# Performance work log

Hardware: AMD Instinct MI355X
Metric: run time of the kernel (lower is better)

## Reference

```python
import jax, jax.numpy as jnp
import numpy as np

N, IN_DIM, OUT_DIM, HEADS, E = 50000, 256, 256, 4, 800000
HEAD_DIM = OUT_DIM // HEADS
NEG_SLOPE = 0.2


def setup_inputs() -> dict:
    key = jax.random.key(0)
    k = jax.random.split(key, 6)
    h = jax.random.normal(k[0], (N, IN_DIM), dtype=jnp.float32)
    edge_index = jax.random.randint(k[1], (2, E), 0, N, dtype=jnp.int32)
    # xavier-uniform-ish scales
    W = jax.random.normal(k[2], (OUT_DIM, IN_DIM), dtype=jnp.float32) * (1.0 / np.sqrt(IN_DIM))
    b = jnp.zeros((OUT_DIM,), dtype=jnp.float32)
    a_src = jax.random.normal(k[3], (HEADS, HEAD_DIM), dtype=jnp.float32) * (1.0 / np.sqrt(HEAD_DIM))
    a_dst = jax.random.normal(k[4], (HEADS, HEAD_DIM), dtype=jnp.float32) * (1.0 / np.sqrt(HEAD_DIM))
    return {"h": h, "edge_index": edge_index, "W": W, "b": b, "a_src": a_src, "a_dst": a_dst}


def reference(h, edge_index, W, b, a_src, a_dst):
    idx_i, idx_j = edge_index[0], edge_index[1]
    Wh = (h @ W.T + b).reshape(N, HEADS, HEAD_DIM)  # [N,H,D]
    # per-node attention logits components (avoids gathering full Wh per edge twice)
    alpha_src = jnp.einsum('nhd,hd->nh', Wh, a_src)  # [N,H]
    alpha_dst = jnp.einsum('nhd,hd->nh', Wh, a_dst)  # [N,H]
    e = jax.nn.leaky_relu(alpha_src[idx_i] + alpha_dst[idx_j], NEG_SLOPE)  # [E,H]
    # segment softmax over neighbors j of each destination row i (sparse.softmax dim=1)
    m = jax.ops.segment_max(e, idx_i, num_segments=N)  # [N,H]
    ex = jnp.exp(e - m[idx_i])
    denom = jax.ops.segment_sum(ex, idx_i, num_segments=N)  # [N,H]
    att = ex / denom[idx_i]  # [E,H]
    # sparse-mm aggregation: out_i = sum_j att_ij * Wh_j, per head
    out = jax.ops.segment_sum(att[:, :, None] * Wh[idx_j], idx_i, num_segments=N)  # [N,H,D]
    return out.reshape(N, OUT_DIM)
```

## Files before the change

kernel.cpp:

```cpp
#include <hip/hip_runtime.h>
#include <hip/hip_bf16.h>
#include <stdint.h>

constexpr int IN_DIM  = 256;
constexpr int OUT_DIM = 256;
constexpr int HEADS   = 4;
constexpr int HEAD_DIM = 64;
constexpr float NEG_SLOPE = 0.2f;

typedef __attribute__((ext_vector_type(8))) short bf16x8;
typedef __attribute__((ext_vector_type(4))) float f32x4;

static __device__ __forceinline__ unsigned short f2bf(float f) {
  union { float f; uint32_t u; } v; v.f = f;
  uint32_t u = v.u;
  return (unsigned short)((u + 0x7fffu + ((u >> 16) & 1u)) >> 16);
}

__global__ __launch_bounds__(256) void k_prep(
    const float* __restrict__ W, const float* __restrict__ b,
    const float* __restrict__ a_src, const float* __restrict__ a_dst,
    float* __restrict__ csrc, unsigned short* __restrict__ Wb,
    int* __restrict__ counts, int* __restrict__ cursor, int N) {
  int bid = blockIdx.x, t = threadIdx.x;
  int i = bid * 256 + t;
  if (i < N) { counts[i] = 0; cursor[i] = 0; }
  if (bid == 0 && t < 8) {
    int hh = t & 3;
    const float* a = (t < 4 ? a_src : a_dst) + hh * HEAD_DIM;
    float cs = 0.f;
    for (int d = 0; d < HEAD_DIM; ++d) cs += b[hh * HEAD_DIM + d] * a[d];
    csrc[t] = cs;
  } else if (bid >= 8 && bid < 40) {
    int base = (bid - 8) * 2048 + t * 8;
    float4 f0 = *(const float4*)(W + base);
    float4 f1 = *(const float4*)(W + base + 4);
    union { unsigned short us[8]; uint4 u4; } pk;
    pk.us[0]=f2bf(f0.x); pk.us[1]=f2bf(f0.y); pk.us[2]=f2bf(f0.z); pk.us[3]=f2bf(f0.w);
    pk.us[4]=f2bf(f1.x); pk.us[5]=f2bf(f1.y); pk.us[6]=f2bf(f1.z); pk.us[7]=f2bf(f1.w);
    *(uint4*)(Wb + base) = pk.u4;
  }
}

__global__ __launch_bounds__(256) void k_gemm_mfma(
    const float* __restrict__ h, const unsigned short* __restrict__ Wb,
    const float* __restrict__ b,
    const float* __restrict__ a_src, const float* __restrict__ a_dst,
    const float* __restrict__ csrc,
    unsigned short* __restrict__ Wh,
    float* __restrict__ asrc, float* __restrict__ adst, int N) {
  __shared__ unsigned short lds[2 * 20480];
  const int t = threadIdx.x;
  const int w = t >> 6, l = t & 63;
  const int lm = l & 15, g = l >> 4;
  const int r0 = blockIdx.x * 64;

  f32x4 acc[4][4];
  const f32x4 fz = {0.f, 0.f, 0.f, 0.f};
#pragma unroll
  for (int fm = 0; fm < 4; ++fm)
#pragma unroll
    for (int fn = 0; fn < 4; ++fn) acc[fm][fn] = fz;

  float breg[4], asg[4], adg[4];
#pragma unroll
  for (int fn = 0; fn < 4; ++fn) {
    breg[fn] = b[w * 64 + fn * 16 + lm];
    asg[fn]  = a_src[w * 64 + fn * 16 + lm];
    adg[fn]  = a_dst[w * 64 + fn * 16 + lm];
  }

  auto stageA = [&](int ch, int s) {
    int k0 = ch * 64;
    int row = t >> 2;
    int grow = r0 + row;
    unsigned short* dstbase = lds + s * 20480 + row * 64;
#pragma unroll
    for (int cc = 0; cc < 2; ++cc) {
      int c = (t & 3) * 2 + cc;
      union { unsigned short us[8]; bf16x8 v; } pk;
      if (grow < N) {
        const float* src = h + (size_t)grow * 256 + k0 + c * 8;
        float4 f0 = *(const float4*)(src);
        float4 f1 = *(const float4*)(src + 4);
        pk.us[0]=f2bf(f0.x); pk.us[1]=f2bf(f0.y); pk.us[2]=f2bf(f0.z); pk.us[3]=f2bf(f0.w);
        pk.us[4]=f2bf(f1.x); pk.us[5]=f2bf(f1.y); pk.us[6]=f2bf(f1.z); pk.us[7]=f2bf(f1.w);
      } else {
#pragma unroll
        for (int e = 0; e < 8; ++e) pk.us[e] = 0;
      }
      *(bf16x8*)(dstbase + ((c ^ (row & 7)) * 8)) = pk.v;
    }
  };

  auto stageB = [&](int ch, int s) {
    int k0 = ch * 64;
    unsigned short* Bbase = lds + s * 20480 + 4096;
    int c  = l & 7;
    int rs = l >> 3;
#pragma unroll
    for (int i = 0; i < 8; ++i) {
      int row = w * 64 + i * 8 + rs;
      bf16x8 v = *(const bf16x8*)(Wb + (size_t)row * 256 + k0 + c * 8);
      *(bf16x8*)(Bbase + row * 64 + ((c ^ rs) * 8)) = v;
    }
  };

  auto compute = [&](int s) {
    const unsigned short* A = lds + s * 20480;
    const unsigned short* B = lds + s * 20480 + 4096;
#pragma unroll
    for (int ks = 0; ks < 2; ++ks) {
      bf16x8 af[4], bfr[4];
#pragma unroll
      for (int fm = 0; fm < 4; ++fm) {
        int row = fm * 16 + lm;
        af[fm] = *(const bf16x8*)(A + row * 64 + (((ks * 4 + g) ^ (row & 7)) * 8));
      }
#pragma unroll
      for (int fn = 0; fn < 4; ++fn) {
        int row = w * 64 + fn * 16 + lm;
        bfr[fn] = *(const bf16x8*)(B + row * 64 + (((ks * 4 + g) ^ (row & 7)) * 8));
      }
#pragma unroll
      for (int fm = 0; fm < 4; ++fm)
#pragma unroll
        for (int fn = 0; fn < 4; ++fn)
          acc[fm][fn] = __builtin_amdgcn_mfma_f32_16x16x32_bf16(
              af[fm], bfr[fn], acc[fm][fn], 0, 0, 0);
    }
  };

  stageA(0, 0); stageB(0, 0);
  __syncthreads();
#pragma unroll
  for (int ch = 0; ch < 4; ++ch) {
    int cur = ch & 1;
    if (ch < 3) { stageA(ch + 1, cur ^ 1); stageB(ch + 1, cur ^ 1); }
    compute(cur);
    __syncthreads();
  }

#pragma unroll
  for (int fm = 0; fm < 4; ++fm) {
#pragma unroll
    for (int r = 0; r < 4; ++r) {
      int grow = r0 + fm * 16 + g * 4 + r;
      if (grow < N) {
        size_t rowoff = (size_t)grow * 256;
#pragma unroll
        for (int fn = 0; fn < 4; ++fn) {
          int col = w * 64 + fn * 16 + lm;
          Wh[rowoff + col] = f2bf(acc[fm][fn][r] + breg[fn]);
        }
      }
    }
  }

  float cs = csrc[w], cd = csrc[4 + w];
#pragma unroll
  for (int fm = 0; fm < 4; ++fm) {
#pragma unroll
    for (int r = 0; r < 4; ++r) {
      float ps = acc[fm][0][r] * asg[0] + acc[fm][1][r] * asg[1]
               + acc[fm][2][r] * asg[2] + acc[fm][3][r] * asg[3];
      float pd = acc[fm][0][r] * adg[0] + acc[fm][1][r] * adg[1]
               + acc[fm][2][r] * adg[2] + acc[fm][3][r] * adg[3];
#pragma unroll
      for (int off = 1; off < 16; off <<= 1) {
        ps += __shfl_xor(ps, off, 64);
        pd += __shfl_xor(pd, off, 64);
      }
      if (lm == 0) {
        int grow = r0 + fm * 16 + g * 4 + r;
        if (grow < N) {
          asrc[grow * 4 + w] = ps + cs;
          adst[grow * 4 + w] = pd + cd;
        }
      }
    }
  }
}

__global__ __launch_bounds__(256) void k_hist(const int* __restrict__ idx_i,
                                              int* __restrict__ counts, int E) {
  int e = blockIdx.x * 256 + threadIdx.x;
  if (e < E) atomicAdd(&counts[idx_i[e]], 1);
}

__global__ __launch_bounds__(256) void k_scanA(const int* __restrict__ counts,
                                               int* __restrict__ offsets,
                                               int* __restrict__ bsum, int N) {
  __shared__ int s[256];
  int t = threadIdx.x;
  int idx = blockIdx.x * 256 + t;
  int v = (idx < N) ? counts[idx] : 0;
  s[t] = v;
  __syncthreads();
  for (int off = 1; off < 256; off <<= 1) {
    int x = (t >= off) ? s[t - off] : 0;
    __syncthreads();
    s[t] += x;
    __syncthreads();
  }
  if (idx < N) offsets[idx] = s[t] - v;
  if (t == 255) bsum[blockIdx.x] = s[255];
}

__global__ __launch_bounds__(256) void k_scanB(int* __restrict__ bsum, int nb) {
  __shared__ int s[256];
  int t = threadIdx.x;
  int v = (t < nb) ? bsum[t] : 0;
  s[t] = v;
  __syncthreads();
  for (int off = 1; off < 256; off <<= 1) {
    int x = (t >= off) ? s[t - off] : 0;
    __syncthreads();
    s[t] += x;
    __syncthreads();
  }
  if (t < nb) bsum[t] = s[t] - v;
}

__global__ __launch_bounds__(256) void k_scanC(int* __restrict__ offsets,
                                               const int* __restrict__ bsum,
                                               int N, int E) {
  int idx = blockIdx.x * 256 + threadIdx.x;
  if (idx < N) offsets[idx] += bsum[blockIdx.x];
  if (idx == 0) offsets[N] = E;
}

__global__ __launch_bounds__(256) void k_scatter(const int* __restrict__ idx_i,
                                                 const int* __restrict__ idx_j,
                                                 const int* __restrict__ offsets,
                                                 int* __restrict__ cursor,
                                                 int* __restrict__ csr_j, int E) {
  int e = blockIdx.x * 256 + threadIdx.x;
  if (e < E) {
    int i = idx_i[e];
    int p = offsets[i] + atomicAdd(&cursor[i], 1);
    csr_j[p] = idx_j[e];
  }
}

__global__ __launch_bounds__(256) void k_aggregate(const int* __restrict__ offsets,
                                                   const int* __restrict__ csr_j,
                                                   const float* __restrict__ asrc,
                                                   const float* __restrict__ adst,
                                                   const unsigned short* __restrict__ Wh,
                                                   float* __restrict__ out, int N) {
  int t = threadIdx.x;
  int wv = t >> 6, l = t & 63;
  int half = l >> 5, ll = l & 31;
  int i = blockIdx.x * 8 + wv * 2 + half;
  bool valid = i < N;
  int beg = valid ? offsets[i] : 0;
  int end = valid ? offsets[i + 1] : 0;
  int deg = end - beg;
  int hh = ll >> 3;
  float aih = valid ? asrc[i * 4 + hh] : 0.f;

  float o[8];
#pragma unroll
  for (int d = 0; d < 8; ++d) o[d] = 0.f;
  float denom = 0.f;

  for (int q = 0; q < deg; q += 8) {
    int jj[8];
    float wgt[8];
    uint4 vv[8];
#pragma unroll
    for (int k = 0; k < 8; ++k) {
      int qk = q + k;
      int qc = qk < deg - 1 ? qk : deg - 1;
      jj[k] = csr_j[beg + qc];
    }
#pragma unroll
    for (int k = 0; k < 8; ++k) {
      float s = aih + adst[(size_t)jj[k] * 4 + hh];
      s = s > 0.f ? s : NEG_SLOPE * s;
      s = (q + k < deg) ? s : -1e38f;
      wgt[k] = __expf(s);
      vv[k] = *(const uint4*)(Wh + (size_t)jj[k] * 256 + ll * 8);
    }
    denom += ((wgt[0] + wgt[1]) + (wgt[2] + wgt[3])) +
             ((wgt[4] + wgt[5]) + (wgt[6] + wgt[7]));
#pragma unroll
    for (int k = 0; k < 8; ++k) {
      union { uint32_t u; float f; } c0, c1, c2, c3, c4, c5, c6, c7;
      c0.u = vv[k].x << 16; c1.u = vv[k].x & 0xffff0000u;
      c2.u = vv[k].y << 16; c3.u = vv[k].y & 0xffff0000u;
      c4.u = vv[k].z << 16; c5.u = vv[k].z & 0xffff0000u;
      c6.u = vv[k].w << 16; c7.u = vv[k].w & 0xffff0000u;
      float wk = wgt[k];
      o[0] += wk * c0.f; o[1] += wk * c1.f;
      o[2] += wk * c2.f; o[3] += wk * c3.f;
      o[4] += wk * c4.f; o[5] += wk * c5.f;
      o[6] += wk * c6.f; o[7] += wk * c7.f;
    }
  }

  if (valid) {
    float inv = (deg > 0) ? 1.f / denom : 0.f;
    float4 o0 = {o[0] * inv, o[1] * inv, o[2] * inv, o[3] * inv};
    float4 o1 = {o[4] * inv, o[5] * inv, o[6] * inv, o[7] * inv};
    float* dst = out + (size_t)i * 256 + ll * 8;
    *(float4*)(dst) = o0;
    *(float4*)(dst + 4) = o1;
  }
}

extern "C" void kernel_launch(void* const* d_in, const int* in_sizes, int n_in,
                              void* d_out, int out_size, void* d_ws, size_t ws_size,
                              hipStream_t stream) {
  const float* h     = (const float*)d_in[0];
  const int*   eidx  = (const int*)  d_in[1];
  const float* W     = (const float*)d_in[2];
  const float* b     = (const float*)d_in[3];
  const float* a_src = (const float*)d_in[4];
  const float* a_dst = (const float*)d_in[5];
  float* out = (float*)d_out;

  const int N = in_sizes[0] / IN_DIM;
  const int E = in_sizes[1] / 2;
  const int* idx_i = eidx;
  const int* idx_j = eidx + E;

  char* p = (char*)d_ws;
  auto alloc = [&](size_t bytes) {
    char* r = p;
    p += (bytes + 255) & ~(size_t)255;
    return r;
  };
  float* csrc = (float*)alloc(8 * sizeof(float));
  unsigned short* Wb = (unsigned short*)alloc((size_t)OUT_DIM * IN_DIM * sizeof(unsigned short));
  unsigned short* Wh = (unsigned short*)alloc((size_t)N * OUT_DIM * sizeof(unsigned short));
  float* asrc = (float*)alloc((size_t)N * HEADS * sizeof(float));
  float* adst = (float*)alloc((size_t)N * HEADS * sizeof(float));
  int* counts  = (int*)alloc((size_t)N * sizeof(int));
  int* offsets = (int*)alloc(((size_t)N + 1) * sizeof(int));
  int* cursor  = (int*)alloc((size_t)N * sizeof(int));
  int* bsum    = (int*)alloc(256 * sizeof(int));
  int* csrj    = (int*)alloc((size_t)E * sizeof(int));

  const int nbN = (N + 255) / 256;
  const int nbE = (E + 255) / 256;

  k_prep<<<nbN, 256, 0, stream>>>(W, b, a_src, a_dst, csrc, Wb, counts, cursor, N);
  k_gemm_mfma<<<(N + 63) / 64, 256, 0, stream>>>(h, Wb, b, a_src, a_dst, csrc,
                                                 Wh, asrc, adst, N);
  k_hist<<<nbE, 256, 0, stream>>>(idx_i, counts, E);
  k_scanA<<<nbN, 256, 0, stream>>>(counts, offsets, bsum, N);
  k_scanB<<<1, 256, 0, stream>>>(bsum, nbN);
  k_scanC<<<nbN, 256, 0, stream>>>(offsets, bsum, N, E);
  k_scatter<<<nbE, 256, 0, stream>>>(idx_i, idx_j, offsets, cursor, csrj, E);
  k_aggregate<<<(N + 7) / 8, 256, 0, stream>>>(offsets, csrj, asrc, adst, Wh, out, N);
}
```

Baseline: 187.2 us.

## Fuse histogram into GEMM, merge scan phases, use offsets as scatter cursor

```diff
diff --git a/kernel.cpp b/kernel.cpp
--- a/kernel.cpp
+++ b/kernel.cpp
@@ -20,25 +20,22 @@
 __global__ __launch_bounds__(256) void k_prep(
     const float* __restrict__ W, const float* __restrict__ b,
     const float* __restrict__ a_src, const float* __restrict__ a_dst,
-    float* __restrict__ csrc, unsigned short* __restrict__ Wb,
-    int* __restrict__ counts, int* __restrict__ cursor, int N) {
+    float* __restrict__ csrc, unsigned short* __restrict__ Wb) {
   int bid = blockIdx.x, t = threadIdx.x;
-  int i = bid * 256 + t;
-  if (i < N) { counts[i] = 0; cursor[i] = 0; }
-  if (bid == 0 && t < 8) {
-    int hh = t & 3;
-    const float* a = (t < 4 ? a_src : a_dst) + hh * HEAD_DIM;
-    float cs = 0.f;
-    for (int d = 0; d < HEAD_DIM; ++d) cs += b[hh * HEAD_DIM + d] * a[d];
-    csrc[t] = cs;
-  } else if (bid >= 8 && bid < 40) {
-    int base = (bid - 8) * 2048 + t * 8;
+  if (bid < 32) {
+    int base = bid * 2048 + t * 8;
     float4 f0 = *(const float4*)(W + base);
     float4 f1 = *(const float4*)(W + base + 4);
     union { unsigned short us[8]; uint4 u4; } pk;
     pk.us[0]=f2bf(f0.x); pk.us[1]=f2bf(f0.y); pk.us[2]=f2bf(f0.z); pk.us[3]=f2bf(f0.w);
     pk.us[4]=f2bf(f1.x); pk.us[5]=f2bf(f1.y); pk.us[6]=f2bf(f1.z); pk.us[7]=f2bf(f1.w);
     *(uint4*)(Wb + base) = pk.u4;
+  } else if (t < 8) {
+    int hh = t & 3;
+    const float* a = (t < 4 ? a_src : a_dst) + hh * HEAD_DIM;
+    float cs = 0.f;
+    for (int d = 0; d < HEAD_DIM; ++d) cs += b[hh * HEAD_DIM + d] * a[d];
+    csrc[t] = cs;
   }
 }
 
@@ -48,7 +45,8 @@
     const float* __restrict__ a_src, const float* __restrict__ a_dst,
     const float* __restrict__ csrc,
     unsigned short* __restrict__ Wh,
-    float* __restrict__ asrc, float* __restrict__ adst, int N) {
+    float* __restrict__ asrc, float* __restrict__ adst,
+    const int* __restrict__ idx_i, int* __restrict__ counts, int N, int E) {
   __shared__ unsigned short lds[2 * 20480];
   const int t = threadIdx.x;
   const int w = t >> 6, l = t & 63;
@@ -80,9 +78,9 @@
       int c = (t & 3) * 2 + cc;
       union { unsigned short us[8]; bf16x8 v; } pk;
       if (grow < N) {
-        const float* src = h + (size_t)grow * 256 + k0 + c * 8;
-        float4 f0 = *(const float4*)(src);
-        float4 f1 = *(const float4*)(src + 4);
+        const f32x4* src = (const f32x4*)(h + (size_t)grow * 256 + k0 + c * 8);
+        f32x4 f0 = __builtin_nontemporal_load(src);
+        f32x4 f1 = __builtin_nontemporal_load(src + 1);
         pk.us[0]=f2bf(f0.x); pk.us[1]=f2bf(f0.y); pk.us[2]=f2bf(f0.z); pk.us[3]=f2bf(f0.w);
         pk.us[4]=f2bf(f1.x); pk.us[5]=f2bf(f1.y); pk.us[6]=f2bf(f1.z); pk.us[7]=f2bf(f1.w);
       } else {
@@ -180,12 +178,14 @@
       }
     }
   }
-}
-
-__global__ __launch_bounds__(256) void k_hist(const int* __restrict__ idx_i,
-                                              int* __restrict__ counts, int E) {
-  int e = blockIdx.x * 256 + threadIdx.x;
-  if (e < E) atomicAdd(&counts[idx_i[e]], 1);
+
+  {
+    long long nb = gridDim.x;
+    long long e0 = (long long)blockIdx.x * E / nb;
+    long long e1 = ((long long)blockIdx.x + 1) * E / nb;
+    for (long long e = e0 + t; e < e1; e += 256)
+      atomicAdd(&counts[idx_i[e]], 1);
+  }
 }
 
 __global__ __launch_bounds__(256) void k_scanA(const int* __restrict__ counts,
@@ -207,7 +207,9 @@
   if (t == 255) bsum[blockIdx.x] = s[255];
 }
 
-__global__ __launch_bounds__(256) void k_scanB(int* __restrict__ bsum, int nb) {
+__global__ __launch_bounds__(256) void k_scanBC(int* __restrict__ offsets,
+                                                const int* __restrict__ bsum,
+                                                int nb, int N) {
   __shared__ int s[256];
   int t = threadIdx.x;
   int v = (t < nb) ? bsum[t] : 0;
@@ -219,26 +221,20 @@
     s[t] += x;
     __syncthreads();
   }
-  if (t < nb) bsum[t] = s[t] - v;
-}
-
-__global__ __launch_bounds__(256) void k_scanC(int* __restrict__ offsets,
-                                               const int* __restrict__ bsum,
-                                               int N, int E) {
-  int idx = blockIdx.x * 256 + threadIdx.x;
-  if (idx < N) offsets[idx] += bsum[blockIdx.x];
-  if (idx == 0) offsets[N] = E;
+  int bid = blockIdx.x;
+  int add = (bid > 0) ? s[bid - 1] : 0;
+  int idx = bid * 256 + t;
+  if (idx < N) offsets[idx] += add;
 }
 
 __global__ __launch_bounds__(256) void k_scatter(const int* __restrict__ idx_i,
                                                  const int* __restrict__ idx_j,
-                                                 const int* __restrict__ offsets,
-                                                 int* __restrict__ cursor,
+                                                 int* __restrict__ offsets,
                                                  int* __restrict__ csr_j, int E) {
   int e = blockIdx.x * 256 + threadIdx.x;
   if (e < E) {
     int i = idx_i[e];
-    int p = offsets[i] + atomicAdd(&cursor[i], 1);
+    int p = atomicAdd(&offsets[i], 1);
     csr_j[p] = idx_j[e];
   }
 }
@@ -254,8 +250,8 @@
   int half = l >> 5, ll = l & 31;
   int i = blockIdx.x * 8 + wv * 2 + half;
   bool valid = i < N;
-  int beg = valid ? offsets[i] : 0;
-  int end = valid ? offsets[i + 1] : 0;
+  int beg = (valid && i > 0) ? offsets[i - 1] : 0;
+  int end = valid ? offsets[i] : 0;
   int deg = end - beg;
   int hh = ll >> 3;
   float aih = valid ? asrc[i * 4 + hh] : 0.f;
@@ -302,11 +298,11 @@
 
   if (valid) {
     float inv = (deg > 0) ? 1.f / denom : 0.f;
-    float4 o0 = {o[0] * inv, o[1] * inv, o[2] * inv, o[3] * inv};
-    float4 o1 = {o[4] * inv, o[5] * inv, o[6] * inv, o[7] * inv};
-    float* dst = out + (size_t)i * 256 + ll * 8;
-    *(float4*)(dst) = o0;
-    *(float4*)(dst + 4) = o1;
+    f32x4 o0 = {o[0] * inv, o[1] * inv, o[2] * inv, o[3] * inv};
+    f32x4 o1 = {o[4] * inv, o[5] * inv, o[6] * inv, o[7] * inv};
+    f32x4* dst = (f32x4*)(out + (size_t)i * 256 + ll * 8);
+    __builtin_nontemporal_store(o0, dst);
+    __builtin_nontemporal_store(o1, dst + 1);
   }
 }
 
@@ -339,20 +335,19 @@
   float* adst = (float*)alloc((size_t)N * HEADS * sizeof(float));
   int* counts  = (int*)alloc((size_t)N * sizeof(int));
   int* offsets = (int*)alloc(((size_t)N + 1) * sizeof(int));
-  int* cursor  = (int*)alloc((size_t)N * sizeof(int));
   int* bsum    = (int*)alloc(256 * sizeof(int));
   int* csrj    = (int*)alloc((size_t)E * sizeof(int));
 
   const int nbN = (N + 255) / 256;
   const int nbE = (E + 255) / 256;
-
-  k_prep<<<nbN, 256, 0, stream>>>(W, b, a_src, a_dst, csrc, Wb, counts, cursor, N);
-  k_gemm_mfma<<<(N + 63) / 64, 256, 0, stream>>>(h, Wb, b, a_src, a_dst, csrc,
-                                                 Wh, asrc, adst, N);
-  k_hist<<<nbE, 256, 0, stream>>>(idx_i, counts, E);
+  const int nbM = (N + 63) / 64;
+
+  (void)hipMemsetAsync(counts, 0, (size_t)N * sizeof(int), stream);
+  k_prep<<<33, 256, 0, stream>>>(W, b, a_src, a_dst, csrc, Wb);
+  k_gemm_mfma<<<nbM, 256, 0, stream>>>(h, Wb, b, a_src, a_dst, csrc,
+                                       Wh, asrc, adst, idx_i, counts, N, E);
   k_scanA<<<nbN, 256, 0, stream>>>(counts, offsets, bsum, N);
-  k_scanB<<<1, 256, 0, stream>>>(bsum, nbN);
-  k_scanC<<<nbN, 256, 0, stream>>>(offsets, bsum, N, E);
-  k_scatter<<<nbE, 256, 0, stream>>>(idx_i, idx_j, offsets, cursor, csrj, E);
+  k_scanBC<<<nbN, 256, 0, stream>>>(offsets, bsum, nbN, N);
+  k_scatter<<<nbE, 256, 0, stream>>>(idx_i, idx_j, offsets, csrj, E);
   k_aggregate<<<(N + 7) / 8, 256, 0, stream>>>(offsets, csrj, asrc, adst, Wh, out, N);
 }
```

Result: slower. 196.7 us (+5.1%).
